# Optimization experiments

Measured on AMD Instinct MI355X. Metric: run time of the kernel, lower is better.

The kernel has to match this reference:

```python
import jax, jax.numpy as jnp
import numpy as np

DIM = 512
NHEADS = 8
HEAD_DIM = DIM // NHEADS
LN_EPS = 1e-5


def _layernorm(x, g, b):
    m = jnp.mean(x, axis=-1, keepdims=True)
    v = jnp.mean((x - m) ** 2, axis=-1, keepdims=True)
    return (x - m) * jax.lax.rsqrt(v + LN_EPS) * g + b


def setup_inputs() -> dict:
    key = jax.random.key(0)
    ks = jax.random.split(key, 12)
    s = 1.0 / np.sqrt(DIM)
    inp = {
        "x": jax.random.normal(ks[0], (4, 2048, DIM), dtype=jnp.float32),
        "Wq": jax.random.uniform(ks[1], (DIM, DIM), jnp.float32, -s, s),
        "bq": jnp.zeros((DIM,), jnp.float32),
        "Wk": jax.random.uniform(ks[2], (DIM, DIM), jnp.float32, -s, s),
        "bk": jnp.zeros((DIM,), jnp.float32),
        "Wv": jax.random.uniform(ks[3], (DIM, DIM), jnp.float32, -s, s),
        "bv": jnp.zeros((DIM,), jnp.float32),
        "Wo": jax.random.uniform(ks[4], (DIM, DIM), jnp.float32, -s, s),
        "bo": jnp.zeros((DIM,), jnp.float32),
        "W1": jax.random.uniform(ks[5], (DIM, 2 * DIM), jnp.float32, -s, s),
        "b1": jnp.zeros((2 * DIM,), jnp.float32),
        "W2": jax.random.uniform(ks[6], (2 * DIM, DIM), jnp.float32, -1.0 / np.sqrt(2 * DIM), 1.0 / np.sqrt(2 * DIM)),
        "b2": jnp.zeros((DIM,), jnp.float32),
        "g1": jnp.ones((DIM,), jnp.float32),
        "be1": jnp.zeros((DIM,), jnp.float32),
        "g2": jnp.ones((DIM,), jnp.float32),
        "be2": jnp.zeros((DIM,), jnp.float32),
    }
    return inp


def reference(x, Wq, bq, Wk, bk, Wv, bv, Wo, bo, W1, b1, W2, b2, g1, be1, g2, be2):
    # norm_before=True path; dropout disabled (inference)
    bsz, n, _ = x.shape
    res = x
    xn = _layernorm(x, g1, be1)

    def proj(W, b):
        return (xn @ W + b).reshape(bsz, n, NHEADS, HEAD_DIM).transpose(0, 2, 1, 3)  # (B,H,N,D)

    q = proj(Wq, bq) / np.sqrt(HEAD_DIM).astype(np.float32)
    k = proj(Wk, bk)
    v = proj(Wv, bv)

    q = jax.nn.elu(q) + 1.0
    k = jax.nn.elu(k) + 1.0

    # quadratic score as in the original module (B,H,N,N)
    score = jnp.einsum("bhnd,bhmd->bhnm", q, k)
    denom = jnp.sum(score, axis=-1, keepdims=True) + 1e-5
    score = score / denom
    out = jnp.einsum("bhnm,bhmd->bhnd", score, v)

    out = out.transpose(0, 2, 1, 3).reshape(bsz, n, DIM)
    out = out @ Wo + bo
    out = res + out

    res2 = out
    h = _layernorm(out, g2, be2)
    h = jax.nn.relu(h @ W1 + b1) @ W2 + b2
    return res2 + h
```

## Files before the change

### kernel.cpp

```cpp
#include <hip/hip_runtime.h>
#include <hip/hip_bf16.h>
#include <math.h>

#define DIM 512
#define HEADS 8
#define HD 64
#define ROWS_TOTAL 8192
#define SEQ 2048
#define NSLICE 16

typedef __hip_bfloat16 bf16;
typedef __bf16 bf16x8 __attribute__((ext_vector_type(8)));
typedef float f32x4 __attribute__((ext_vector_type(4)));

__device__ __forceinline__ float elu1(float x) {
    return x > 0.f ? x + 1.f : __expf(x);
}
__device__ __forceinline__ void gl16(const void* g, void* l) {
    __builtin_amdgcn_global_load_lds(
        (const __attribute__((address_space(1))) void*)g,
        (__attribute__((address_space(3))) void*)l, 16, 0, 0);
}
__device__ __forceinline__ unsigned short f2bu(float v) {
    bf16 t = __float2bfloat16(v);
    return *(unsigned short*)&t;
}

__global__ __launch_bounds__(256) void prep_kernel(
    const float* __restrict__ Wq, const float* __restrict__ Wk,
    const float* __restrict__ Wv, const float* __restrict__ Wo,
    const float* __restrict__ W1, const float* __restrict__ W2,
    bf16* WqkvT, bf16* WoT, bf16* W1T, bf16* W2T,
    const float* __restrict__ x, const float* __restrict__ g,
    const float* __restrict__ b, bf16* __restrict__ xout)
{
    __shared__ float t[32][33];
    int bx = blockIdx.x;
    if (bx >= 2048) {
        int row  = (bx - 2048) * 4 + (threadIdx.x >> 6);
        int lane = threadIdx.x & 63;
        const float* xr = x + (size_t)row * DIM + lane * 8;
        float4 v1 = *(const float4*)xr;
        float4 v2 = *(const float4*)(xr + 4);
        float f[8] = {v1.x, v1.y, v1.z, v1.w, v2.x, v2.y, v2.z, v2.w};
        float s = 0.f, sq = 0.f;
#pragma unroll
        for (int j = 0; j < 8; ++j) { s += f[j]; sq += f[j]*f[j]; }
#pragma unroll
        for (int off = 32; off > 0; off >>= 1) {
            s  += __shfl_xor(s,  off, 64);
            sq += __shfl_xor(sq, off, 64);
        }
        float mean = s * (1.f / DIM);
        float var  = sq * (1.f / DIM) - mean * mean;
        float rstd = rsqrtf(var + 1e-5f);
        int c = lane * 8;
        float4 ga = *(const float4*)(g + c);
        float4 gb = *(const float4*)(g + c + 4);
        float4 ba = *(const float4*)(b + c);
        float4 bb = *(const float4*)(b + c + 4);
        float gg[8]  = {ga.x,ga.y,ga.z,ga.w,gb.x,gb.y,gb.z,gb.w};
        float bbv[8] = {ba.x,ba.y,ba.z,ba.w,bb.x,bb.y,bb.z,bb.w};
        bf16 ob[8];
#pragma unroll
        for (int j = 0; j < 8; ++j)
            ob[j] = __float2bfloat16((f[j] - mean) * rstd * gg[j] + bbv[j]);
        *(uint4*)(xout + (size_t)row * DIM + c) = *(uint4*)ob;
        return;
    }
    const float* W; bf16* T; int K, N, tk, tn, mode = 0;
    if (bx < 1024) {
        int m = bx >> 8, tix = bx & 255;
        const float* ws_[4] = {Wq, Wk, Wv, Wo};
        W = ws_[m];
        T = (m == 3) ? WoT : WqkvT;
        mode = (m == 1) ? 1 : (m == 2 ? 2 : 0);
        K = 512; N = 512; tn = tix & 15; tk = tix >> 4;
    } else if (bx < 1536) {
        int tix = bx - 1024; W = W1; T = W1T; K = 512; N = 1024; tn = tix & 31; tk = tix >> 5;
    } else {
        int tix = bx - 1536; W = W2; T = W2T; K = 1024; N = 512; tn = tix & 15; tk = tix >> 4;
    }
    int n0 = tn * 32, k0 = tk * 32;
    int tx = threadIdx.x & 31, ty = threadIdx.x >> 5;
#pragma unroll
    for (int i = 0; i < 32; i += 8)
        t[ty + i][tx] = W[(size_t)(k0 + ty + i) * N + n0 + tx];
    __syncthreads();
#pragma unroll
    for (int i = 0; i < 32; i += 8) {
        int n = n0 + ty + i;
        int dr = n;
        if (mode == 1)      dr = 512 + ((n >> 6) << 7) + (n & 63);
        else if (mode == 2) dr = 576 + ((n >> 6) << 7) + (n & 63);
        T[(size_t)dr * K + k0 + tx] = __float2bfloat16(t[tx][ty + i]);
    }
}

__global__ __launch_bounds__(256) void ln_kernel(const bf16* __restrict__ xv,
                                                 const float* __restrict__ g,
                                                 const float* __restrict__ b,
                                                 bf16* __restrict__ out)
{
    int row  = blockIdx.x * 4 + (threadIdx.x >> 6);
    int lane = threadIdx.x & 63;
    bf16x8 v = *(const bf16x8*)(xv + (size_t)row * DIM + lane * 8);
    float f[8];
#pragma unroll
    for (int j = 0; j < 8; ++j) f[j] = (float)v[j];
    float s = 0.f, sq = 0.f;
#pragma unroll
    for (int j = 0; j < 8; ++j) { s += f[j]; sq += f[j]*f[j]; }
#pragma unroll
    for (int off = 32; off > 0; off >>= 1) {
        s  += __shfl_xor(s,  off, 64);
        sq += __shfl_xor(sq, off, 64);
    }
    float mean = s * (1.f / DIM);
    float var  = sq * (1.f / DIM) - mean * mean;
    float rstd = rsqrtf(var + 1e-5f);
    int c = lane * 8;
    float4 ga = *(const float4*)(g + c);
    float4 gb = *(const float4*)(g + c + 4);
    float4 ba = *(const float4*)(b + c);
    float4 bb = *(const float4*)(b + c + 4);
    float gg[8]  = {ga.x,ga.y,ga.z,ga.w,gb.x,gb.y,gb.z,gb.w};
    float bbv[8] = {ba.x,ba.y,ba.z,ba.w,bb.x,bb.y,bb.z,bb.w};
    bf16 ob[8];
#pragma unroll
    for (int j = 0; j < 8; ++j)
        ob[j] = __float2bfloat16((f[j] - mean) * rstd * gg[j] + bbv[j]);
    *(uint4*)(out + (size_t)row * DIM + c) = *(uint4*)ob;
}

__global__ __launch_bounds__(256) void qkv_kv_kernel(
    const bf16* __restrict__ A, const bf16* __restrict__ Bt,
    const float* __restrict__ bq, const float* __restrict__ bk,
    const float* __restrict__ bv, bf16* __restrict__ Qb,
    float* __restrict__ KVTp, float* __restrict__ KSp, float scale)
{
    constexpr int K = 512;
    __shared__ __align__(16) bf16 As[2][128 * 64];
    __shared__ __align__(16) bf16 Bs[2][128 * 64];
    int tid = threadIdx.x;
    int lane = tid & 63, wid = tid >> 6;
    int wr = wid >> 1, wc = wid & 1;
    int cpx = gridDim.x >> 3;
    int work = (blockIdx.x & 7) * cpx + (blockIdx.x >> 3);
    int bx = work % 12, by = work / 12;
    int m0 = by * 128, n0 = bx * 128;
    int sr = tid >> 3, sc = (tid & 7) * 8;
    const bf16* ga = A  + (size_t)(m0 + sr) * K + sc;
    const bf16* gb = Bt + (size_t)(n0 + sr) * K + sc;
    f32x4 acc[4][4] = {};
    int la = lane & 15, ka = lane >> 4;

#pragma unroll
    for (int j = 0; j < 4; ++j) {
        gl16(ga + (size_t)j * 32 * K, &As[0][tid * 8 + j * 2048]);
        gl16(gb + (size_t)j * 32 * K, &Bs[0][tid * 8 + j * 2048]);
    }
    __syncthreads();
    for (int t = 0; t < 8; ++t) {
        int cur = t & 1;
        if (t + 1 < 8) {
            int k0 = (t + 1) << 6;
#pragma unroll
            for (int j = 0; j < 4; ++j) {
                gl16(ga + (size_t)j * 32 * K + k0, &As[cur ^ 1][tid * 8 + j * 2048]);
                gl16(gb + (size_t)j * 32 * K + k0, &Bs[cur ^ 1][tid * 8 + j * 2048]);
            }
        }
        bf16x8 a[2][4], b[2][4];
#pragma unroll
        for (int kk = 0; kk < 2; ++kk) {
#pragma unroll
            for (int m = 0; m < 4; ++m)
                a[kk][m] = *(const bf16x8*)&As[cur][(wr * 64 + m * 16 + la) * 64 + kk * 32 + ka * 8];
#pragma unroll
            for (int n = 0; n < 4; ++n)
                b[kk][n] = *(const bf16x8*)&Bs[cur][(wc * 64 + n * 16 + la) * 64 + kk * 32 + ka * 8];
        }
#pragma unroll
        for (int kk = 0; kk < 2; ++kk)
#pragma unroll
            for (int m = 0; m < 4; ++m)
#pragma unroll
                for (int n = 0; n < 4; ++n)
                    acc[m][n] = __builtin_amdgcn_mfma_f32_16x16x32_bf16(a[kk][m], b[kk][n], acc[m][n], 0, 0, 0);
        __syncthreads();
    }

    int rg = (lane >> 4) * 4;
    if (bx < 4) {
#pragma unroll
        for (int m = 0; m < 4; ++m) {
            int gm = m0 + wr * 64 + m * 16 + rg;
#pragma unroll
            for (int n = 0; n < 4; ++n) {
                int gnl = bx * 128 + wc * 64 + n * 16 + la;
                float bv_ = bq[gnl];
#pragma unroll
                for (int j = 0; j < 4; ++j) {
                    float v = elu1((acc[m][n][j] + bv_) * scale);
                    Qb[(size_t)(gm + j) * 512 + gnl] = __float2bfloat16(v);
                }
            }
        }
    } else {
        int hh = bx - 4;
        int bb = m0 >> 11, sl = (m0 >> 7) & 15;
        int bh = bb * 8 + hh;
        bf16* KT = (bf16*)As;
        bf16* VT = KT + 8192;
        const float* bias = (wc == 0) ? (bk + hh * 64) : (bv + hh * 64);
        bf16* base = (wc == 0) ? KT : VT;
#pragma unroll
        for (int m = 0; m < 4; ++m) {
            int r0 = wr * 64 + m * 16 + rg;
#pragma unroll
            for (int n = 0; n < 4; ++n) {
                int col = n * 16 + la;
                float bv_ = bias[col];
                ushort4 pk;
                unsigned short* pp = (unsigned short*)&pk;
#pragma unroll
                for (int j = 0; j < 4; ++j) {
                    float v = acc[m][n][j] + bv_;
                    if (wc == 0) v = elu1(v);
                    pp[j] = f2bu(v);
                }
                int byteoff = col * 256 + ((r0 * 2) ^ ((col & 7) << 4));
                *(ushort4*)((char*)base + byteoff) = pk;
            }
        }
        __syncthreads();
        f32x4 acc2[4] = {};
        int fe = wid;
#pragma unroll
        for (int kk = 0; kk < 4; ++kk) {
            int kbyte = kk * 64 + ka * 16;
            int ar = fe * 16 + la;
            bf16x8 av = *(const bf16x8*)((char*)VT + ar * 256 + (kbyte ^ ((ar & 7) << 4)));
#pragma unroll
            for (int fd = 0; fd < 4; ++fd) {
                int br = fd * 16 + la;
                bf16x8 bk8 = *(const bf16x8*)((char*)KT + br * 256 + (kbyte ^ ((br & 7) << 4)));
                acc2[fd] = __builtin_amdgcn_mfma_f32_16x16x32_bf16(av, bk8, acc2[fd], 0, 0, 0);
            }
        }
        float* dst = KVTp + (size_t)(bh * 16 + sl) * 4096;
#pragma unroll
        for (int fd = 0; fd < 4; ++fd)
#pragma unroll
            for (int j = 0; j < 4; ++j)
                dst[(fe * 16 + rg + j) * 64 + fd * 16 + la] = acc2[fd][j];
        if (tid < 64) {
            float s = 0.f;
#pragma unroll
            for (int rc = 0; rc < 16; ++rc) {
                bf16x8 kv8 = *(const bf16x8*)((char*)KT + tid * 256 + ((rc * 16) ^ ((tid & 7) << 4)));
#pragma unroll
                for (int j = 0; j < 8; ++j) s += (float)kv8[j];
            }
            KSp[(size_t)(bh * 16 + sl) * 64 + tid] = s;
        }
    }
}

template<int BM, int BN, int EPI>
__global__ __launch_bounds__(256) void mfma_gemm(
    const bf16* __restrict__ A, const bf16* __restrict__ Bt,
    const float* __restrict__ b0, const void* __restrict__ resid,
    void* __restrict__ O0, int N, int K, int GX)
{
    constexpr int MW = BM / 32;
    constexpr int NW = BN / 32;
    __shared__ __align__(16) bf16 As[2][BM * 64];
    __shared__ __align__(16) bf16 Bs[2][BN * 64];
    int tid = threadIdx.x;
    int lane = tid & 63, wid = tid >> 6;
    int wr = wid >> 1, wc = wid & 1;
    int cpx = gridDim.x >> 3;
    int work = (blockIdx.x & 7) * cpx + (blockIdx.x >> 3);
    int bx = work % GX, by = work / GX;
    int m0 = by * BM, n0 = bx * BN;
    int sr = tid >> 3, sc = (tid & 7) * 8;
    const bf16* ga = A  + (size_t)(m0 + sr) * K + sc;
    const bf16* gb = Bt + (size_t)(n0 + sr) * K + sc;
    f32x4 acc[MW][NW] = {};
    int la = lane & 15, ka = lane >> 4;
    int nt = K >> 6;

#pragma unroll
    for (int j = 0; j < MW; ++j)
        gl16(ga + (size_t)j * 32 * K, &As[0][tid * 8 + j * 2048]);
#pragma unroll
    for (int j = 0; j < NW; ++j)
        gl16(gb + (size_t)j * 32 * K, &Bs[0][tid * 8 + j * 2048]);
    __syncthreads();

    for (int t = 0; t < nt; ++t) {
        int cur = t & 1;
        if (t + 1 < nt) {
            int k0 = (t + 1) << 6;
#pragma unroll
            for (int j = 0; j < MW; ++j)
                gl16(ga + (size_t)j * 32 * K + k0, &As[cur ^ 1][tid * 8 + j * 2048]);
#pragma unroll
            for (int j = 0; j < NW; ++j)
                gl16(gb + (size_t)j * 32 * K + k0, &Bs[cur ^ 1][tid * 8 + j * 2048]);
        }
        bf16x8 a[2][MW], b[2][NW];
#pragma unroll
        for (int kk = 0; kk < 2; ++kk) {
#pragma unroll
            for (int m = 0; m < MW; ++m)
                a[kk][m] = *(const bf16x8*)&As[cur][(wr * (BM/2) + m * 16 + la) * 64 + kk * 32 + ka * 8];
#pragma unroll
            for (int n = 0; n < NW; ++n)
                b[kk][n] = *(const bf16x8*)&Bs[cur][(wc * (BN/2) + n * 16 + la) * 64 + kk * 32 + ka * 8];
        }
#pragma unroll
        for (int kk = 0; kk < 2; ++kk)
#pragma unroll
            for (int m = 0; m < MW; ++m)
#pragma unroll
                for (int n = 0; n < NW; ++n)
                    acc[m][n] = __builtin_amdgcn_mfma_f32_16x16x32_bf16(a[kk][m], b[kk][n], acc[m][n], 0, 0, 0);
        __syncthreads();
    }

    int rg = (lane >> 4) * 4;
#pragma unroll
    for (int m = 0; m < MW; ++m) {
        int gm = m0 + wr * (BM/2) + m * 16 + rg;
#pragma unroll
        for (int n = 0; n < NW; ++n) {
            int gn = n0 + wc * (BN/2) + n * 16 + la;
            float bv_ = b0[gn];
#pragma unroll
            for (int j = 0; j < 4; ++j) {
                float v = acc[m][n][j] + bv_;
                if (EPI == 3) v = fmaxf(v, 0.f);
                if (EPI == 0 && resid)
                    v += (float)((const bf16*)resid)[(size_t)(gm + j) * N + gn];
                if (EPI == 2 && resid)
                    v += ((const float*)resid)[(size_t)(gm + j) * N + gn];
                if (EPI == 0) ((float*)O0)[(size_t)(gm + j) * N + gn] = v;
                else          ((bf16*)O0)[(size_t)(gm + j) * N + gn] = __float2bfloat16(v);
            }
        }
    }
}

__global__ __launch_bounds__(256) void attn_gemm(
    const bf16* __restrict__ Q, const float* __restrict__ KVTp,
    const float* __restrict__ KSp, bf16* __restrict__ out)
{
    __shared__ __align__(16) bf16 As[128][72];
    __shared__ __align__(16) bf16 Bs[64][72];
    __shared__ float ks[64];
    __shared__ float dn[128];
    int h = blockIdx.x;
    int m0 = blockIdx.y * 128;
    int bh = ((m0 >> 11) << 3) + h;
    int tid = threadIdx.x;
    int lane = tid & 63, wid = tid >> 6;
    {
        int r = tid >> 3, c0 = (tid & 7) * 8;
#pragma unroll
        for (int p = 0; p < 4; ++p) {
            int row = p * 32 + r;
            *(bf16x8*)&As[row][c0] =
                *(const bf16x8*)(Q + (size_t)(m0 + row) * DIM + h * HD + c0);
        }
        const float* kvb = KVTp + (size_t)bh * 16 * 4096;
        int e = tid & 63, d0 = (tid >> 6) * 16;
        float s_[16] = {};
#pragma unroll
        for (int sl = 0; sl < NSLICE; ++sl) {
            const float* p = kvb + sl * 4096 + e * 64 + d0;
#pragma unroll
            for (int i = 0; i < 16; ++i) s_[i] += p[i];
        }
#pragma unroll
        for (int i = 0; i < 16; ++i)
            Bs[e][d0 + i] = __float2bfloat16(s_[i]);
        if (tid < 64) {
            float s = 0.f;
#pragma unroll
            for (int sl = 0; sl < NSLICE; ++sl)
                s += KSp[(size_t)(bh * 16 + sl) * 64 + tid];
            ks[tid] = s;
        }
    }
    __syncthreads();
    if (tid < 128) {
        float s = 0.f;
#pragma unroll
        for (int c = 0; c < 8; ++c) {
            bf16x8 qv = *(const bf16x8*)&As[tid][c * 8];
#pragma unroll
            for (int j = 0; j < 8; ++j)
                s += (float)qv[j] * ks[c * 8 + j];
        }
        dn[tid] = 1.f / (s + 1e-5f);
    }
    int la = lane & 15, ka = lane >> 4;
    f32x4 acc[2][4] = {};
#pragma unroll
    for (int s = 0; s < 2; ++s) {
        bf16x8 a[2], b[4];
#pragma unroll
        for (int m = 0; m < 2; ++m)
            a[m] = *(const bf16x8*)&As[wid * 32 + m * 16 + la][s * 32 + ka * 8];
#pragma unroll
        for (int n = 0; n < 4; ++n)
            b[n] = *(const bf16x8*)&Bs[n * 16 + la][s * 32 + ka * 8];
#pragma unroll
        for (int m = 0; m < 2; ++m)
#pragma unroll
            for (int n = 0; n < 4; ++n)
                acc[m][n] = __builtin_amdgcn_mfma_f32_16x16x32_bf16(a[m], b[n], acc[m][n], 0, 0, 0);
    }
    __syncthreads();
    int rg = (lane >> 4) * 4;
#pragma unroll
    for (int m = 0; m < 2; ++m) {
#pragma unroll
        for (int j = 0; j < 4; ++j) {
            int lr = wid * 32 + m * 16 + rg + j;
            float rdn = dn[lr];
            int gm = m0 + lr;
#pragma unroll
            for (int n = 0; n < 4; ++n) {
                int gn = h * HD + n * 16 + la;
                out[(size_t)gm * DIM + gn] = __float2bfloat16(acc[m][n][j] * rdn);
            }
        }
    }
}

extern "C" void kernel_launch(void* const* d_in, const int* in_sizes, int n_in,
                              void* d_out, int out_size, void* d_ws, size_t ws_size,
                              hipStream_t stream)
{
    const float* x   = (const float*)d_in[0];
    const float* Wq  = (const float*)d_in[1];
    const float* bq  = (const float*)d_in[2];
    const float* Wk  = (const float*)d_in[3];
    const float* bk  = (const float*)d_in[4];
    const float* Wv  = (const float*)d_in[5];
    const float* bv  = (const float*)d_in[6];
    const float* Wo  = (const float*)d_in[7];
    const float* bo  = (const float*)d_in[8];
    const float* W1  = (const float*)d_in[9];
    const float* b1  = (const float*)d_in[10];
    const float* W2  = (const float*)d_in[11];
    const float* b2  = (const float*)d_in[12];
    const float* g1  = (const float*)d_in[13];
    const float* be1 = (const float*)d_in[14];
    const float* g2  = (const float*)d_in[15];
    const float* be2 = (const float*)d_in[16];

    char* wsb = (char*)d_ws;
    const size_t MB = 1u << 20;
    bf16*  Qb  = (bf16*)(wsb + 0 * MB);
    bf16*  xn  = (bf16*)(wsb + 8 * MB);
    bf16*  yb  = (bf16*)(wsb + 16 * MB);
    bf16*  hb  = (bf16*)(wsb + 24 * MB);
    bf16*  WqkvT = (bf16*)(wsb + 32 * MB);
    bf16*  WoT = WqkvT + 1536 * 512;
    bf16*  W1T = WoT + 512 * 512;
    bf16*  W2T = W1T + 1024 * 512;
    float* KVTp = (float*)(wsb + 40 * MB);
    float* KSp  = (float*)(wsb + 48 * MB);
    bf16*  F1  = (bf16*)(wsb + 0 * MB);
    bf16*  attnb = xn;

    float* out = (float*)d_out;
    dim3 blk(256);

    prep_kernel<<<4096, blk, 0, stream>>>(Wq, Wk, Wv, Wo, W1, W2,
                                          WqkvT, WoT, W1T, W2T, x, g1, be1, xn);
    qkv_kv_kernel<<<768, blk, 0, stream>>>(xn, WqkvT, bq, bk, bv,
                                           Qb, KVTp, KSp, 0.125f);
    attn_gemm<<<dim3(8, 64), blk, 0, stream>>>(Qb, KVTp, KSp, attnb);
    mfma_gemm<64, 64, 2><<<1024, blk, 0, stream>>>(
        attnb, WoT, bo, x, yb, 512, 512, 8);
    ln_kernel<<<2048, blk, 0, stream>>>(yb, g2, be2, hb);
    mfma_gemm<64, 64, 3><<<2048, blk, 0, stream>>>(
        hb, W1T, b1, nullptr, F1, 1024, 512, 16);
    mfma_gemm<64, 64, 0><<<1024, blk, 0, stream>>>(
        F1, W2T, b2, yb, out, 512, 1024, 8);
}
```

Before: 137.1 us.

## Swizzle LDS tiles with XOR pattern and keep bf16 residual copy of input

The GEMM kernels now load global tiles into LDS with an XOR-swizzled column offset and read MFMA fragments with the matching swizzle. This is meant to remove LDS bank conflicts on the 128-byte row stride. Separately, the prep kernel writes a bf16 copy of x, and the Wo GEMM reads that as its residual instead of fp32 x, which halves residual read traffic. The cost is an extra 8 MB bf16 write and a loss of precision in the first residual.

```diff
diff --git a/kernel.cpp b/kernel.cpp
--- a/kernel.cpp
+++ b/kernel.cpp
@@ -32,7 +32,8 @@
     const float* __restrict__ W1, const float* __restrict__ W2,
     bf16* WqkvT, bf16* WoT, bf16* W1T, bf16* W2T,
     const float* __restrict__ x, const float* __restrict__ g,
-    const float* __restrict__ b, bf16* __restrict__ xout)
+    const float* __restrict__ b, bf16* __restrict__ xout,
+    bf16* __restrict__ xb)
 {
     __shared__ float t[32][33];
     int bx = blockIdx.x;
@@ -43,6 +44,11 @@
         float4 v1 = *(const float4*)xr;
         float4 v2 = *(const float4*)(xr + 4);
         float f[8] = {v1.x, v1.y, v1.z, v1.w, v2.x, v2.y, v2.z, v2.w};
+        int c = lane * 8;
+        bf16 rb[8];
+#pragma unroll
+        for (int j = 0; j < 8; ++j) rb[j] = __float2bfloat16(f[j]);
+        *(uint4*)(xb + (size_t)row * DIM + c) = *(uint4*)rb;
         float s = 0.f, sq = 0.f;
 #pragma unroll
         for (int j = 0; j < 8; ++j) { s += f[j]; sq += f[j]*f[j]; }
@@ -54,7 +60,6 @@
         float mean = s * (1.f / DIM);
         float var  = sq * (1.f / DIM) - mean * mean;
         float rstd = rsqrtf(var + 1e-5f);
-        int c = lane * 8;
         float4 ga = *(const float4*)(g + c);
         float4 gb = *(const float4*)(g + c + 4);
         float4 ba = *(const float4*)(b + c);
@@ -149,11 +154,13 @@
     int work = (blockIdx.x & 7) * cpx + (blockIdx.x >> 3);
     int bx = work % 12, by = work / 12;
     int m0 = by * 128, n0 = bx * 128;
-    int sr = tid >> 3, sc = (tid & 7) * 8;
-    const bf16* ga = A  + (size_t)(m0 + sr) * K + sc;
-    const bf16* gb = Bt + (size_t)(n0 + sr) * K + sc;
+    int sr = tid >> 3;
+    int scb = (((tid & 7) << 4) ^ ((sr & 7) << 4)) >> 1;
+    const bf16* ga = A  + (size_t)(m0 + sr) * K + scb;
+    const bf16* gb = Bt + (size_t)(n0 + sr) * K + scb;
     f32x4 acc[4][4] = {};
     int la = lane & 15, ka = lane >> 4;
+    int xo = (la & 7) << 4;
 
 #pragma unroll
     for (int j = 0; j < 4; ++j) {
@@ -171,15 +178,18 @@
                 gl16(gb + (size_t)j * 32 * K + k0, &Bs[cur ^ 1][tid * 8 + j * 2048]);
             }
         }
+        const char* Ab = (const char*)As[cur];
+        const char* Bb = (const char*)Bs[cur];
         bf16x8 a[2][4], b[2][4];
 #pragma unroll
         for (int kk = 0; kk < 2; ++kk) {
+            int kb = (kk * 64 + ka * 16) ^ xo;
 #pragma unroll
             for (int m = 0; m < 4; ++m)
-                a[kk][m] = *(const bf16x8*)&As[cur][(wr * 64 + m * 16 + la) * 64 + kk * 32 + ka * 8];
+                a[kk][m] = *(const bf16x8*)(Ab + (wr * 64 + m * 16 + la) * 128 + kb);
 #pragma unroll
             for (int n = 0; n < 4; ++n)
-                b[kk][n] = *(const bf16x8*)&Bs[cur][(wc * 64 + n * 16 + la) * 64 + kk * 32 + ka * 8];
+                b[kk][n] = *(const bf16x8*)(Bb + (wc * 64 + n * 16 + la) * 128 + kb);
         }
 #pragma unroll
         for (int kk = 0; kk < 2; ++kk)
@@ -271,7 +281,7 @@
 template<int BM, int BN, int EPI>
 __global__ __launch_bounds__(256) void mfma_gemm(
     const bf16* __restrict__ A, const bf16* __restrict__ Bt,
-    const float* __restrict__ b0, const void* __restrict__ resid,
+    const float* __restrict__ b0, const bf16* __restrict__ resid,
     void* __restrict__ O0, int N, int K, int GX)
 {
     constexpr int MW = BM / 32;
@@ -285,11 +295,13 @@
     int work = (blockIdx.x & 7) * cpx + (blockIdx.x >> 3);
     int bx = work % GX, by = work / GX;
     int m0 = by * BM, n0 = bx * BN;
-    int sr = tid >> 3, sc = (tid & 7) * 8;
-    const bf16* ga = A  + (size_t)(m0 + sr) * K + sc;
-    const bf16* gb = Bt + (size_t)(n0 + sr) * K + sc;
+    int sr = tid >> 3;
+    int scb = (((tid & 7) << 4) ^ ((sr & 7) << 4)) >> 1;
+    const bf16* ga = A  + (size_t)(m0 + sr) * K + scb;
+    const bf16* gb = Bt + (size_t)(n0 + sr) * K + scb;
     f32x4 acc[MW][NW] = {};
     int la = lane & 15, ka = lane >> 4;
+    int xo = (la & 7) << 4;
     int nt = K >> 6;
 
 #pragma unroll
@@ -311,15 +323,18 @@
             for (int j = 0; j < NW; ++j)
                 gl16(gb + (size_t)j * 32 * K + k0, &Bs[cur ^ 1][tid * 8 + j * 2048]);
         }
+        const char* Ab = (const char*)As[cur];
+        const char* Bb = (const char*)Bs[cur];
         bf16x8 a[2][MW], b[2][NW];
 #pragma unroll
         for (int kk = 0; kk < 2; ++kk) {
+            int kb = (kk * 64 + ka * 16) ^ xo;
 #pragma unroll
             for (int m = 0; m < MW; ++m)
-                a[kk][m] = *(const bf16x8*)&As[cur][(wr * (BM/2) + m * 16 + la) * 64 + kk * 32 + ka * 8];
+                a[kk][m] = *(const bf16x8*)(Ab + (wr * (BM/2) + m * 16 + la) * 128 + kb);
 #pragma unroll
             for (int n = 0; n < NW; ++n)
-                b[kk][n] = *(const bf16x8*)&Bs[cur][(wc * (BN/2) + n * 16 + la) * 64 + kk * 32 + ka * 8];
+                b[kk][n] = *(const bf16x8*)(Bb + (wc * (BN/2) + n * 16 + la) * 128 + kb);
         }
 #pragma unroll
         for (int kk = 0; kk < 2; ++kk)
@@ -343,10 +358,8 @@
             for (int j = 0; j < 4; ++j) {
                 float v = acc[m][n][j] + bv_;
                 if (EPI == 3) v = fmaxf(v, 0.f);
-                if (EPI == 0 && resid)
-                    v += (float)((const bf16*)resid)[(size_t)(gm + j) * N + gn];
-                if (EPI == 2 && resid)
-                    v += ((const float*)resid)[(size_t)(gm + j) * N + gn];
+                if ((EPI == 0 || EPI == 2) && resid)
+                    v += (float)resid[(size_t)(gm + j) * N + gn];
                 if (EPI == 0) ((float*)O0)[(size_t)(gm + j) * N + gn] = v;
                 else          ((bf16*)O0)[(size_t)(gm + j) * N + gn] = __float2bfloat16(v);
             }
@@ -476,6 +489,7 @@
     bf16*  W2T = W1T + 1024 * 512;
     float* KVTp = (float*)(wsb + 40 * MB);
     float* KSp  = (float*)(wsb + 48 * MB);
+    bf16*  xb   = (bf16*)(wsb + 49 * MB);
     bf16*  F1  = (bf16*)(wsb + 0 * MB);
     bf16*  attnb = xn;
 
@@ -483,12 +497,12 @@
     dim3 blk(256);
 
     prep_kernel<<<4096, blk, 0, stream>>>(Wq, Wk, Wv, Wo, W1, W2,
-                                          WqkvT, WoT, W1T, W2T, x, g1, be1, xn);
+                                          WqkvT, WoT, W1T, W2T, x, g1, be1, xn, xb);
     qkv_kv_kernel<<<768, blk, 0, stream>>>(xn, WqkvT, bq, bk, bv,
                                            Qb, KVTp, KSp, 0.125f);
     attn_gemm<<<dim3(8, 64), blk, 0, stream>>>(Qb, KVTp, KSp, attnb);
     mfma_gemm<64, 64, 2><<<1024, blk, 0, stream>>>(
-        attnb, WoT, bo, x, yb, 512, 512, 8);
+        attnb, WoT, bo, xb, yb, 512, 512, 8);
     ln_kernel<<<2048, blk, 0, stream>>>(yb, g2, be2, hb);
     mfma_gemm<64, 64, 3><<<2048, blk, 0, stream>>>(
         hb, W1T, b1, nullptr, F1, 1024, 512, 16);
```

Measured after the change: 120.6 us. 12.0% less time.
